# Kernel optimization log

Measured on AMD Instinct MI355X. Metric: run time of the kernel, lower is better.

## Reference

```python
import jax, jax.numpy as jnp
import numpy as np

B, L, D_IN = 16384, 28, 256
LATENT, HID = 128, 256
STEP = 0.5  # odeint rk4 step_size
N_STEPS = 2 * (L - 1)  # 54 fixed-grid steps covering t in [0, 27]


def setup_inputs() -> dict:
    key = jax.random.key(0)
    ks = jax.random.split(key, 20)
    s = 0.1  # init std used in ODEFunc; reuse for all params for simplicity
    p = {}
    p["trajectory"] = jax.random.normal(ks[0], (B, L, D_IN), dtype=jnp.float32)
    # encoder: Linear(3*D_IN -> HID), Linear(HID -> LATENT)
    p["We1"] = jax.random.normal(ks[1], (HID, 3 * D_IN)) * s
    p["be1"] = jnp.zeros((HID,))
    p["We2"] = jax.random.normal(ks[2], (LATENT, HID)) * s
    p["be2"] = jnp.zeros((LATENT,))
    # ODEFunc time embed: Linear(1 -> LATENT) -> vector form
    p["wte"] = jax.random.normal(ks[3], (LATENT,)) * s
    p["bte"] = jnp.zeros((LATENT,))
    # ODEFunc net: LATENT -> HID -> HID -> LATENT
    p["W1"] = jax.random.normal(ks[4], (HID, LATENT)) * s
    p["b1"] = jnp.zeros((HID,))
    p["W2"] = jax.random.normal(ks[5], (HID, HID)) * s
    p["b2"] = jnp.zeros((HID,))
    p["W3"] = jax.random.normal(ks[6], (LATENT, HID)) * s
    p["b3"] = jnp.zeros((LATENT,))
    # classifier: LATENT -> HID -> 1
    p["Wc1"] = jax.random.normal(ks[7], (HID, LATENT)) * s
    p["bc1"] = jnp.zeros((HID,))
    p["Wc2"] = jax.random.normal(ks[8], (1, HID)) * s
    p["bc2"] = jnp.zeros((1,))
    return p


def _forward(trajectory, We1, be1, We2, be2, wte, bte, W1, b1, W2, b2, W3, b3,
             Wc1, bc1, Wc2, bc2):
    bsz = trajectory.shape[0]
    # encoder (eval mode: dropout is identity)
    x0 = trajectory[:, :3, :].reshape(bsz, -1)  # [B, 3*D_IN]
    h = jax.nn.relu(x0 @ We1.T + be1)
    z0 = h @ We2.T + be2  # [B, LATENT]

    def f(t, z):
        # z + time embedding, then 3-layer tanh MLP
        zt = z + (t * wte + bte)
        h1 = jnp.tanh(zt @ W1.T + b1)
        h2 = jnp.tanh(h1 @ W2.T + b2)
        return h2 @ W3.T + b3

    def rk4_step(z, n):
        # torchdiffeq 'rk4' fixed-grid = 3/8-rule RK4
        t = n.astype(z.dtype) * STEP
        dt = jnp.asarray(STEP, z.dtype)
        k1 = f(t, z)
        k2 = f(t + dt / 3, z + dt * k1 / 3)
        k3 = f(t + 2 * dt / 3, z + dt * (k2 - k1 / 3))
        k4 = f(t + dt, z + dt * (k1 - k2 + k3))
        z_new = z + dt * (k1 + 3 * (k2 + k3) + k4) / 8
        return z_new, z_new

    _, zs = jax.lax.scan(rk4_step, z0, jnp.arange(N_STEPS))  # [54, B, LATENT]
    # output grid t = 0,1,...,27: z0 plus every second substep state
    z_trajectory = jnp.concatenate([z0[None], zs[1::2]], axis=0)  # [28, B, LATENT]

    zL = z_trajectory[-1]
    hc = jax.nn.relu(zL @ Wc1.T + bc1)
    prob = jax.nn.sigmoid(hc @ Wc2.T + bc2)  # [B, 1]
    return prob, z_trajectory


def reference(trajectory, We1, be1, We2, be2, wte, bte, W1, b1, W2, b2, W3, b3,
              Wc1, bc1, Wc2, bc2):
    return _forward(trajectory, We1, be1, We2, be2, wte, bte, W1, b1, W2, b2,
                    W3, b3, Wc1, bc1, Wc2, bc2)
```

## Files before the change

### kernel.cpp

```cpp
#include <hip/hip_runtime.h>
#include <cstdint>
#include <cstddef>

#define DEV __device__ __forceinline__

typedef float  f32x2  __attribute__((ext_vector_type(2)));
typedef float  f32x4  __attribute__((ext_vector_type(4)));
typedef float  f32x16 __attribute__((ext_vector_type(16)));
typedef int    i32x2  __attribute__((ext_vector_type(2)));
typedef int    i32x4  __attribute__((ext_vector_type(4)));
typedef _Float16 f16x2 __attribute__((ext_vector_type(2)));
typedef _Float16 f16x8 __attribute__((ext_vector_type(8)));

constexpr float DT   = 0.5f;
constexpr float DT3  = 0.5f / 3.0f;
constexpr float DT23 = 1.0f / 3.0f;
constexpr float DT8  = 0.0625f;

constexpr float S5  = 32.0f,   IS5 = 1.0f / 32.0f;
constexpr float S6  = 64.0f,   IS6 = 1.0f / 64.0f;
constexpr float S8  = 256.0f,  IS8 = 1.0f / 256.0f;
constexpr float S11 = 2048.0f;

constexpr int ACT  = 0;
constexpr int SLO  = 16384;
constexpr int ALO  = 32768;
constexpr int W2L  = 49152;
constexpr int W3L  = 114688;
constexpr int B2O  = 147456;
constexpr int B3O  = 148480;
constexpr int U01O = 148992;
constexpr int SMEM_BYTES = 151040;

#define MFMA16(a, b, c) __builtin_amdgcn_mfma_f32_32x32x16_f16((a), (b), (c), 0, 0, 0)

DEV int swzb(int off, int m) { return off ^ ((m & 7) << 4); }

DEV float tanh_fast(float x) {
  float e = __builtin_amdgcn_exp2f(x * 2.885390082f);
  return 1.0f - 2.0f * __builtin_amdgcn_rcpf(e + 1.0f);
}

DEV unsigned pkh2(float a, float b) {
  f16x2 p = { (_Float16)a, (_Float16)b };
  return __builtin_bit_cast(unsigned, p);
}

DEV f16x8 read_f16t(const char* buf, int RS, int m, int kelem) {
  return *(const f16x8*)(buf + swzb(m * RS + kelem * 2, m));
}
DEV i32x2 read8b(const char* buf, int m, int kelem) {
  return *(const i32x2*)(buf + swzb(m * 256 + kelem, m));
}
DEV f16x8 mulh(f16x8 v, float s) {
  _Float16 h = (_Float16)s;
  f16x8 r;
#pragma unroll
  for (int j = 0; j < 8; ++j) r[j] = v[j] * h;
  return r;
}
DEV f16x8 dec8(i32x2 r, float sc) {
  f32x2 p0 = __builtin_amdgcn_cvt_pk_f32_fp8(r[0], false);
  f32x2 p1 = __builtin_amdgcn_cvt_pk_f32_fp8(r[0], true);
  f32x2 p2 = __builtin_amdgcn_cvt_pk_f32_fp8(r[1], false);
  f32x2 p3 = __builtin_amdgcn_cvt_pk_f32_fp8(r[1], true);
  f16x2 q0 = __builtin_bit_cast(f16x2, __builtin_amdgcn_cvt_pkrtz(p0[0] * sc, p0[1] * sc));
  f16x2 q1 = __builtin_bit_cast(f16x2, __builtin_amdgcn_cvt_pkrtz(p1[0] * sc, p1[1] * sc));
  f16x2 q2 = __builtin_bit_cast(f16x2, __builtin_amdgcn_cvt_pkrtz(p2[0] * sc, p2[1] * sc));
  f16x2 q3 = __builtin_bit_cast(f16x2, __builtin_amdgcn_cvt_pkrtz(p3[0] * sc, p3[1] * sc));
  f16x8 o;
  o[0] = q0[0]; o[1] = q0[1]; o[2] = q1[0]; o[3] = q1[1];
  o[4] = q2[0]; o[5] = q2[1]; o[6] = q3[0]; o[7] = q3[1];
  return o;
}
DEV int pk4fp8(float a, float b, float c, float d) {
  int w = __builtin_amdgcn_cvt_pk_fp8_f32(a, b, 0, false);
  w = __builtin_amdgcn_cvt_pk_fp8_f32(c, d, w, true);
  return w;
}

DEV void cvt_hl_s(const float* p, f16x8& hi, f16x8& lo, float ls) {
  f32x4 a = *(const f32x4*)p;
  f32x4 b = *(const f32x4*)(p + 4);
#pragma unroll
  for (int j = 0; j < 4; ++j) {
    _Float16 h = (_Float16)a[j]; hi[j] = h; lo[j] = (_Float16)((a[j] - (float)h) * ls);
    _Float16 g = (_Float16)b[j]; hi[4 + j] = g; lo[4 + j] = (_Float16)((b[j] - (float)g) * ls);
  }
}
DEV f16x8 cvt_h(const float* p) {
  f32x4 a = *(const f32x4*)p;
  f32x4 b = *(const f32x4*)(p + 4);
  f16x8 hi;
#pragma unroll
  for (int j = 0; j < 4; ++j) { hi[j] = (_Float16)a[j]; hi[4 + j] = (_Float16)b[j]; }
  return hi;
}
DEV f16x8 cvt8v(f32x4 a, f32x4 b) {
  f16x8 h;
#pragma unroll
  for (int j = 0; j < 4; ++j) { h[j] = (_Float16)a[j]; h[4 + j] = (_Float16)b[j]; }
  return h;
}

DEV void write_h8(char* hi, char* lo, f32x16 acc[2][2], int lane, int nbase) {
  const int mr = lane & 31, hh = lane >> 5;
#pragma unroll
  for (int nt = 0; nt < 2; ++nt)
#pragma unroll
    for (int mt = 0; mt < 2; ++mt) {
      int m = mt * 32 + mr;
#pragma unroll
      for (int g = 0; g < 4; ++g) {
        int n = nbase + nt * 32 + 8 * g + 4 * hh;
        float v0 = tanh_fast(acc[nt][mt][4 * g + 0]);
        float v1 = tanh_fast(acc[nt][mt][4 * g + 1]);
        float v2 = tanh_fast(acc[nt][mt][4 * g + 2]);
        float v3 = tanh_fast(acc[nt][mt][4 * g + 3]);
        i32x2 w;
        w[0] = (int)pkh2(v0, v1);
        w[1] = (int)pkh2(v2, v3);
        *(i32x2*)(hi + swzb(m * 512 + n * 2, m)) = w;
        float l0 = (v0 - (float)(_Float16)v0) * S11;
        float l1 = (v1 - (float)(_Float16)v1) * S11;
        float l2 = (v2 - (float)(_Float16)v2) * S11;
        float l3 = (v3 - (float)(_Float16)v3) * S11;
        *(int*)(lo + swzb(m * 256 + n, m)) = pk4fp8(l0, l1, l2, l3);
      }
    }
}

DEV void write_h16(char* hi, char* lo, f32x16 acc[2][2], int lane, int nbase, float ls) {
  const int mr = lane & 31, hh = lane >> 5;
#pragma unroll
  for (int nt = 0; nt < 2; ++nt)
#pragma unroll
    for (int mt = 0; mt < 2; ++mt) {
      int m = mt * 32 + mr;
#pragma unroll
      for (int g = 0; g < 4; ++g) {
        int n = nbase + nt * 32 + 8 * g + 4 * hh;
        float v0 = fmaxf(acc[nt][mt][4 * g + 0], 0.f);
        float v1 = fmaxf(acc[nt][mt][4 * g + 1], 0.f);
        float v2 = fmaxf(acc[nt][mt][4 * g + 2], 0.f);
        float v3 = fmaxf(acc[nt][mt][4 * g + 3], 0.f);
        i32x2 w;
        w[0] = (int)pkh2(v0, v1); w[1] = (int)pkh2(v2, v3);
        *(i32x2*)(hi + swzb(m * 512 + n * 2, m)) = w;
        w[0] = (int)pkh2((v0 - (float)(_Float16)v0) * ls, (v1 - (float)(_Float16)v1) * ls);
        w[1] = (int)pkh2((v2 - (float)(_Float16)v2) * ls, (v3 - (float)(_Float16)v3) * ls);
        *(i32x2*)(lo + swzb(m * 512 + n * 2, m)) = w;
      }
    }
}

DEV void write_hc(char* hi, f32x16 acc[2][2], int lane, int nbase) {
  const int mr = lane & 31, hh = lane >> 5;
#pragma unroll
  for (int nt = 0; nt < 2; ++nt)
#pragma unroll
    for (int mt = 0; mt < 2; ++mt) {
      int m = mt * 32 + mr;
#pragma unroll
      for (int g = 0; g < 4; ++g) {
        int n = nbase + nt * 32 + 8 * g + 4 * hh;
        i32x2 w;
        w[0] = (int)pkh2(fmaxf(acc[nt][mt][4 * g + 0], 0.f), fmaxf(acc[nt][mt][4 * g + 1], 0.f));
        w[1] = (int)pkh2(fmaxf(acc[nt][mt][4 * g + 2], 0.f), fmaxf(acc[nt][mt][4 * g + 3], 0.f));
        *(i32x2*)(hi + swzb(m * 512 + n * 2, m)) = w;
      }
    }
}

DEV void write_f32v(char* dst, const f32x16& a0, const f32x16& a1, int lane, int nbase) {
  const int mr = lane & 31, hh = lane >> 5;
#pragma unroll
  for (int mt = 0; mt < 2; ++mt) {
    const f32x16& a = mt ? a1 : a0;
    int m = mt * 32 + mr;
#pragma unroll
    for (int g = 0; g < 4; ++g) {
      int n = nbase + 8 * g + 4 * hh;
      f32x4 v = { a[4 * g + 0], a[4 * g + 1], a[4 * g + 2], a[4 * g + 3] };
      *(f32x4*)(dst + swzb(m * 512 + n * 4, m)) = v;
    }
  }
}

DEV void read_kv(const char* sm, int m, int cs, float* kv) {
#pragma unroll
  for (int blk = 0; blk < 8; ++blk) {
    f32x4 v = *(const f32x4*)(sm + ACT + swzb(m * 512 + cs * 128 + blk * 16, m));
    kv[4 * blk] = v[0]; kv[4 * blk + 1] = v[1]; kv[4 * blk + 2] = v[2]; kv[4 * blk + 3] = v[3];
  }
}

DEV void write_stage8(char* sm, int m, int cs, int gg, const float* sv) {
  i32x4 wh, wl;
#pragma unroll
  for (int j = 0; j < 4; ++j) {
    float v0 = sv[2 * j], v1 = sv[2 * j + 1];
    _Float16 h0 = (_Float16)v0, h1 = (_Float16)v1;
    f16x2 ph = { h0, h1 };
    f16x2 pl = { (_Float16)((v0 - (float)h0) * S5), (_Float16)((v1 - (float)h1) * S5) };
    wh[j] = __builtin_bit_cast(int, ph);
    wl[j] = __builtin_bit_cast(int, pl);
  }
  int off = swzb(m * 256 + cs * 64 + gg * 16, m);
  *(i32x4*)(sm + ACT + off) = wh;
  *(i32x4*)(sm + SLO + off) = wl;
}

DEV void f_eval(char* sm, const f16x8* wsW1, float t,
                const f16x8* W1h, const f16x8* Au,
                const float* __restrict__ W2, const float* __restrict__ W3,
                int lane, int wave) {
  const int mr = lane & 31, kh = (lane >> 5) * 8, hh = lane >> 5;
  const int wb64 = wave * 64, wb32 = wave * 32;

  __syncthreads();
  f32x16 a1[2][2];
#pragma unroll
  for (int nt = 0; nt < 2; ++nt)
#pragma unroll
    for (int mt = 0; mt < 2; ++mt)
#pragma unroll
      for (int r = 0; r < 16; ++r) a1[nt][mt][r] = 0.f;

  const f16x8* wp = wsW1 + (size_t)wave * 1024 + lane;
  f16x8 wq[2][2];
  wq[0][0] = wp[0];   wq[0][1] = wp[512];
  wq[1][0] = wp[64];  wq[1][1] = wp[512 + 64];
#pragma unroll
  for (int ks = 0; ks < 8; ++ks) {
    f16x8 wl0 = wq[ks & 1][0], wl1 = wq[ks & 1][1];
    if (ks + 2 < 8) {
      wq[ks & 1][0] = wp[(ks + 2) * 64];
      wq[ks & 1][1] = wp[512 + (ks + 2) * 64];
    }
    int ke = ks * 16 + kh;
    f16x8 bh0 = read_f16t(sm + ACT, 256, mr, ke);
    f16x8 bh1 = read_f16t(sm + ACT, 256, 32 + mr, ke);
    f16x8 bl0 = read_f16t(sm + SLO, 256, mr, ke);
    f16x8 bl1 = read_f16t(sm + SLO, 256, 32 + mr, ke);
    f16x8 bh0m = mulh(bh0, IS8), bh1m = mulh(bh1, IS8);
    f16x8 w1s0 = mulh(W1h[ks], IS5), w1s1 = mulh(W1h[8 + ks], IS5);
    a1[0][0] = MFMA16(W1h[ks],     bh0, a1[0][0]);
    a1[0][1] = MFMA16(W1h[ks],     bh1, a1[0][1]);
    a1[1][0] = MFMA16(W1h[8 + ks], bh0, a1[1][0]);
    a1[1][1] = MFMA16(W1h[8 + ks], bh1, a1[1][1]);
    a1[0][0] = MFMA16(w1s0, bl0, a1[0][0]);
    a1[0][1] = MFMA16(w1s0, bl1, a1[0][1]);
    a1[1][0] = MFMA16(w1s1, bl0, a1[1][0]);
    a1[1][1] = MFMA16(w1s1, bl1, a1[1][1]);
    a1[0][0] = MFMA16(wl0, bh0m, a1[0][0]);
    a1[0][1] = MFMA16(wl0, bh1m, a1[0][1]);
    a1[1][0] = MFMA16(wl1, bh0m, a1[1][0]);
    a1[1][1] = MFMA16(wl1, bh1m, a1[1][1]);
  }
  {
    _Float16 th = (_Float16)t;
    _Float16 tl = (_Float16)(t - (float)th);
    f16x8 ub, ul;
#pragma unroll
    for (int j = 0; j < 8; ++j) { ub[j] = (_Float16)0.f; ul[j] = (_Float16)0.f; }
    if (kh == 0) {
      ub[0] = (_Float16)1.0f; ub[1] = th;
      ub[2] = (_Float16)IS8;  ub[3] = (_Float16)((float)th * IS8);
      ul[1] = tl;             ul[3] = (_Float16)((float)tl * IS8);
    }
#pragma unroll
    for (int nt = 0; nt < 2; ++nt) {
      a1[nt][0] = MFMA16(Au[nt], ub, a1[nt][0]);
      a1[nt][1] = MFMA16(Au[nt], ub, a1[nt][1]);
      a1[nt][0] = MFMA16(Au[nt], ul, a1[nt][0]);
      a1[nt][1] = MFMA16(Au[nt], ul, a1[nt][1]);
    }
  }
  __syncthreads();
  write_h8(sm + ACT, sm + ALO, a1, lane, wb64);
  __syncthreads();

  const float* B2p = (const float*)(sm + B2O);
  f32x16 a2[2][2];
#pragma unroll
  for (int nt = 0; nt < 2; ++nt)
#pragma unroll
    for (int g = 0; g < 4; ++g) {
      int n = wb64 + nt * 32 + 8 * g + 4 * hh;
      f32x4 bv = *(const f32x4*)(B2p + n);
#pragma unroll
      for (int r = 0; r < 4; ++r) { a2[nt][0][4 * g + r] = bv[r]; a2[nt][1][4 * g + r] = bv[r]; }
    }
  const float* w2r0 = W2 + (size_t)(wb64 + mr) * 256 + kh;
  const float* w2r1 = W2 + (size_t)(wb64 + 32 + mr) * 256 + kh;
  f32x4 w2b[2][2][2];
#pragma unroll
  for (int s = 0; s < 2; ++s) {
    w2b[s][0][0] = *(const f32x4*)(w2r0 + s * 16);
    w2b[s][0][1] = *(const f32x4*)(w2r0 + s * 16 + 4);
    w2b[s][1][0] = *(const f32x4*)(w2r1 + s * 16);
    w2b[s][1][1] = *(const f32x4*)(w2r1 + s * 16 + 4);
  }
#pragma unroll
  for (int ks = 0; ks < 16; ++ks) {
    f16x8 W2h0 = cvt8v(w2b[ks & 1][0][0], w2b[ks & 1][0][1]);
    f16x8 W2h1 = cvt8v(w2b[ks & 1][1][0], w2b[ks & 1][1][1]);
    if (ks + 2 < 16) {
      w2b[ks & 1][0][0] = *(const f32x4*)(w2r0 + (ks + 2) * 16);
      w2b[ks & 1][0][1] = *(const f32x4*)(w2r0 + (ks + 2) * 16 + 4);
      w2b[ks & 1][1][0] = *(const f32x4*)(w2r1 + (ks + 2) * 16);
      w2b[ks & 1][1][1] = *(const f32x4*)(w2r1 + (ks + 2) * 16 + 4);
    }
    int ke = ks * 16 + kh;
    f16x8 bh0 = read_f16t(sm + ACT, 512, mr, ke);
    f16x8 bh1 = read_f16t(sm + ACT, 512, 32 + mr, ke);
    f16x8 bl0 = dec8(read8b(sm + ALO, mr, ke), IS6);
    f16x8 bl1 = dec8(read8b(sm + ALO, 32 + mr, ke), IS6);
    f16x8 w2s0 = mulh(W2h0, IS5), w2s1 = mulh(W2h1, IS5);
    f16x8 bh0m = mulh(bh0, IS6), bh1m = mulh(bh1, IS6);
    i32x2 t0 = *(const i32x2*)(sm + W2L + ((size_t)((wave * 2 + 0) * 16 + ks) * 64 + lane) * 8);
    i32x2 t1 = *(const i32x2*)(sm + W2L + ((size_t)((wave * 2 + 1) * 16 + ks) * 64 + lane) * 8);
    f16x8 wa0 = dec8(t0, IS5), wa1 = dec8(t1, IS5);
    a2[0][0] = MFMA16(W2h0, bh0, a2[0][0]);
    a2[0][1] = MFMA16(W2h0, bh1, a2[0][1]);
    a2[1][0] = MFMA16(W2h1, bh0, a2[1][0]);
    a2[1][1] = MFMA16(W2h1, bh1, a2[1][1]);
    a2[0][0] = MFMA16(w2s0, bl0, a2[0][0]);
    a2[0][1] = MFMA16(w2s0, bl1, a2[0][1]);
    a2[1][0] = MFMA16(w2s1, bl0, a2[1][0]);
    a2[1][1] = MFMA16(w2s1, bl1, a2[1][1]);
    a2[0][0] = MFMA16(wa0, bh0m, a2[0][0]);
    a2[0][1] = MFMA16(wa0, bh1m, a2[0][1]);
    a2[1][0] = MFMA16(wa1, bh0m, a2[1][0]);
    a2[1][1] = MFMA16(wa1, bh1m, a2[1][1]);
  }
  __syncthreads();
  write_h8(sm + ACT, sm + ALO, a2, lane, wb64);
  __syncthreads();

  const float* B3p = (const float*)(sm + B3O);
  f32x16 a30, a31;
#pragma unroll
  for (int g = 0; g < 4; ++g) {
    int n = wb32 + 8 * g + 4 * hh;
    f32x4 bv = *(const f32x4*)(B3p + n);
#pragma unroll
    for (int r = 0; r < 4; ++r) { a30[4 * g + r] = bv[r]; a31[4 * g + r] = bv[r]; }
  }
  const float* w3r = W3 + (size_t)(wb32 + mr) * 256 + kh;
  f32x4 w3b[2][2];
#pragma unroll
  for (int s = 0; s < 2; ++s) {
    w3b[s][0] = *(const f32x4*)(w3r + s * 16);
    w3b[s][1] = *(const f32x4*)(w3r + s * 16 + 4);
  }
#pragma unroll
  for (int ks = 0; ks < 16; ++ks) {
    f16x8 W3h = cvt8v(w3b[ks & 1][0], w3b[ks & 1][1]);
    if (ks + 2 < 16) {
      w3b[ks & 1][0] = *(const f32x4*)(w3r + (ks + 2) * 16);
      w3b[ks & 1][1] = *(const f32x4*)(w3r + (ks + 2) * 16 + 4);
    }
    int ke = ks * 16 + kh;
    f16x8 bh0 = read_f16t(sm + ACT, 512, mr, ke);
    f16x8 bh1 = read_f16t(sm + ACT, 512, 32 + mr, ke);
    f16x8 bl0 = dec8(read8b(sm + ALO, mr, ke), IS6);
    f16x8 bl1 = dec8(read8b(sm + ALO, 32 + mr, ke), IS6);
    f16x8 w3s = mulh(W3h, IS5);
    f16x8 bh0m = mulh(bh0, IS6), bh1m = mulh(bh1, IS6);
    i32x2 t0 = *(const i32x2*)(sm + W3L + ((size_t)(wave * 16 + ks) * 64 + lane) * 8);
    f16x8 wa = dec8(t0, IS5);
    a30 = MFMA16(W3h, bh0, a30);
    a31 = MFMA16(W3h, bh1, a31);
    a30 = MFMA16(w3s, bl0, a30);
    a31 = MFMA16(w3s, bl1, a31);
    a30 = MFMA16(wa, bh0m, a30);
    a31 = MFMA16(wa, bh1m, a31);
  }
  __syncthreads();
  write_f32v(sm + ACT, a30, a31, lane, wb32);
  __syncthreads();
}

__global__ void prep_w1lo(const float* __restrict__ W1, _Float16* __restrict__ ws) {
  int i = blockIdx.x * 256 + threadIdx.x;
  int lane = i & 63, ks = (i >> 6) & 7, nt = (i >> 9) & 1, wave = (i >> 10) & 3;
  int row = wave * 64 + nt * 32 + (lane & 31);
  int col = ks * 16 + (lane >> 5) * 8;
  const float* p = W1 + (size_t)row * 128 + col;
  _Float16* o = ws + (size_t)i * 8;
#pragma unroll
  for (int j = 0; j < 8; ++j) {
    float w = p[j];
    _Float16 h = (_Float16)w;
    o[j] = (_Float16)((w - (float)h) * S8);
  }
}

__global__ __launch_bounds__(256, 1) void node_kernel(
    const float* __restrict__ traj,
    const float* __restrict__ We1, const float* __restrict__ be1,
    const float* __restrict__ We2, const float* __restrict__ be2,
    const float* __restrict__ wte, const float* __restrict__ bte,
    const float* __restrict__ W1,  const float* __restrict__ b1,
    const float* __restrict__ W2,  const float* __restrict__ b2,
    const float* __restrict__ W3,  const float* __restrict__ b3,
    const float* __restrict__ Wc1, const float* __restrict__ bc1,
    const float* __restrict__ Wc2, const float* __restrict__ bc2,
    const _Float16* __restrict__ wsW1h, float* __restrict__ out) {
  __shared__ __align__(16) char sm[SMEM_BYTES];
  const int tid  = threadIdx.x;
  const int lane = tid & 63, wave = tid >> 6;
  const int mr = lane & 31, kh = (lane >> 5) * 8, hh = lane >> 5;
  const int wb64 = wave * 64, wb32 = wave * 32;
  const int brow = blockIdx.x * 64;
  const f16x8* wsW1 = (const f16x8*)wsW1h;

  {
    int n = tid;
    float u0 = b1[n], u1 = 0.f;
    const float* wr = W1 + n * 128;
    for (int k = 0; k < 128; ++k) { float w = wr[k]; u1 += wte[k] * w; u0 += bte[k] * w; }
    float* U = (float*)(sm + U01O);
    U[2 * n] = u0; U[2 * n + 1] = u1;
    ((float*)(sm + B2O))[n] = b2[n];
    if (n < 128) ((float*)(sm + B3O))[n] = b3[n];
  }

  f16x8 W1h[16], Au[2];
#pragma unroll
  for (int nt = 0; nt < 2; ++nt)
#pragma unroll
    for (int ks = 0; ks < 8; ++ks)
      W1h[nt * 8 + ks] = cvt_h(W1 + (size_t)(wb64 + nt * 32 + mr) * 128 + ks * 16 + kh);

  __syncthreads();

#pragma unroll
  for (int nt = 0; nt < 2; ++nt) {
    f16x8 a;
#pragma unroll
    for (int j = 0; j < 8; ++j) a[j] = (_Float16)0.f;
    if (kh == 0) {
      const float* U = (const float*)(sm + U01O);
      int n = wb64 + nt * 32 + mr;
      float u0 = U[2 * n], u1 = U[2 * n + 1];
      _Float16 u0h = (_Float16)u0, u1h = (_Float16)u1;
      a[0] = u0h; a[1] = u1h;
      a[2] = (_Float16)((u0 - (float)u0h) * S8);
      a[3] = (_Float16)((u1 - (float)u1h) * S8);
    }
    Au[nt] = a;
  }

  const int m_own = tid >> 2, cs = tid & 3;

  f32x16 ae[2][2];
#pragma unroll
  for (int nt = 0; nt < 2; ++nt)
#pragma unroll
    for (int mt = 0; mt < 2; ++mt)
#pragma unroll
      for (int r = 0; r < 16; ++r) ae[nt][mt][r] = 0.f;

  for (int c = 0; c < 3; ++c) {
#pragma unroll
    for (int g = 0; g < 8; ++g) {
      const float* xp = traj + (size_t)(brow + m_own) * 7168 + c * 256 + cs * 64 + g * 8;
      f32x4 a = *(const f32x4*)xp;
      f32x4 b = *(const f32x4*)(xp + 4);
      i32x4 wh, wl;
#pragma unroll
      for (int j = 0; j < 2; ++j) {
        float v0 = a[2 * j], v1 = a[2 * j + 1];
        _Float16 h0 = (_Float16)v0, h1 = (_Float16)v1;
        f16x2 ph = { h0, h1 };
        f16x2 pl = { (_Float16)((v0 - (float)h0) * S6), (_Float16)((v1 - (float)h1) * S6) };
        wh[j] = __builtin_bit_cast(int, ph); wl[j] = __builtin_bit_cast(int, pl);
        float w0 = b[2 * j], w1 = b[2 * j + 1];
        _Float16 g0 = (_Float16)w0, g1 = (_Float16)w1;
        f16x2 qh = { g0, g1 };
        f16x2 ql = { (_Float16)((w0 - (float)g0) * S6), (_Float16)((w1 - (float)g1) * S6) };
        wh[2 + j] = __builtin_bit_cast(int, qh); wl[2 + j] = __builtin_bit_cast(int, ql);
      }
      int off = swzb(m_own * 512 + cs * 128 + g * 16, m_own);
      *(i32x4*)(sm + ACT + off) = wh;
      *(i32x4*)(sm + W2L + off) = wl;
    }
    __syncthreads();
#pragma unroll
    for (int ks = 0; ks < 16; ++ks) {
      int ke = ks * 16 + kh;
      f16x8 bh0 = read_f16t(sm + ACT, 512, mr, ke);
      f16x8 bh1 = read_f16t(sm + ACT, 512, 32 + mr, ke);
      f16x8 bl0 = read_f16t(sm + W2L, 512, mr, ke);
      f16x8 bl1 = read_f16t(sm + W2L, 512, 32 + mr, ke);
      f16x8 bh0m = mulh(bh0, IS6), bh1m = mulh(bh1, IS6);
#pragma unroll
      for (int nt = 0; nt < 2; ++nt) {
        f16x8 wh, wl;
        cvt_hl_s(We1 + (size_t)(wb64 + nt * 32 + mr) * 768 + c * 256 + ks * 16 + kh, wh, wl, S6);
        f16x8 whs = mulh(wh, IS6);
        ae[nt][0] = MFMA16(wh, bh0, ae[nt][0]);
        ae[nt][1] = MFMA16(wh, bh1, ae[nt][1]);
        ae[nt][0] = MFMA16(whs, bl0, ae[nt][0]);
        ae[nt][1] = MFMA16(whs, bl1, ae[nt][1]);
        ae[nt][0] = MFMA16(wl, bh0m, ae[nt][0]);
        ae[nt][1] = MFMA16(wl, bh1m, ae[nt][1]);
      }
    }
    __syncthreads();
  }
#pragma unroll
  for (int nt = 0; nt < 2; ++nt)
#pragma unroll
    for (int r = 0; r < 16; ++r) {
      int n = wb64 + nt * 32 + (r & 3) + 8 * (r >> 2) + 4 * hh;
      float bv = be1[n];
      ae[nt][0][r] += bv; ae[nt][1][r] += bv;
    }
  write_h16(sm + ACT, sm + W2L, ae, lane, wb64, S6);
  __syncthreads();

  {
    f32x16 az0, az1;
#pragma unroll
    for (int r = 0; r < 16; ++r) { az0[r] = 0.f; az1[r] = 0.f; }
#pragma unroll
    for (int ks = 0; ks < 16; ++ks) {
      int ke = ks * 16 + kh;
      f16x8 bh0 = read_f16t(sm + ACT, 512, mr, ke);
      f16x8 bh1 = read_f16t(sm + ACT, 512, 32 + mr, ke);
      f16x8 bl0 = read_f16t(sm + W2L, 512, mr, ke);
      f16x8 bl1 = read_f16t(sm + W2L, 512, 32 + mr, ke);
      f16x8 bh0m = mulh(bh0, IS6), bh1m = mulh(bh1, IS6);
      f16x8 wh, wl;
      cvt_hl_s(We2 + (size_t)(wb32 + mr) * 256 + ks * 16 + kh, wh, wl, S6);
      f16x8 whs = mulh(wh, IS6);
      az0 = MFMA16(wh, bh0, az0);
      az1 = MFMA16(wh, bh1, az1);
      az0 = MFMA16(whs, bl0, az0);
      az1 = MFMA16(whs, bl1, az1);
      az0 = MFMA16(wl, bh0m, az0);
      az1 = MFMA16(wl, bh1m, az1);
    }
#pragma unroll
    for (int r = 0; r < 16; ++r) {
      int n = wb32 + (r & 3) + 8 * (r >> 2) + 4 * hh;
      float bv = be2[n];
      az0[r] += bv; az1[r] += bv;
    }
    __syncthreads();
    write_f32v(sm + ACT, az0, az1, lane, wb32);
    __syncthreads();
  }

  float z[32], Acc[32], k1v[32], kv[32];
  read_kv(sm, m_own, cs, z);
  float* outz = out + 16384;
  {
    float* p = outz + (size_t)(brow + m_own) * 128 + cs * 32;
#pragma unroll
    for (int g = 0; g < 8; ++g) {
      f32x4 v = { z[4 * g], z[4 * g + 1], z[4 * g + 2], z[4 * g + 3] };
      *(f32x4*)(p + 4 * g) = v;
    }
  }

#pragma unroll
  for (int nt = 0; nt < 2; ++nt)
    for (int ks = 0; ks < 16; ++ks) {
      const float* p = W2 + (size_t)(wb64 + nt * 32 + mr) * 256 + ks * 16 + kh;
      float l[8];
#pragma unroll
      for (int j = 0; j < 8; ++j) { float w = p[j]; l[j] = (w - (float)(_Float16)w) * S11; }
      i32x2 wv;
      wv[0] = pk4fp8(l[0], l[1], l[2], l[3]);
      wv[1] = pk4fp8(l[4], l[5], l[6], l[7]);
      *(i32x2*)(sm + W2L + ((size_t)((wave * 2 + nt) * 16 + ks) * 64 + lane) * 8) = wv;
    }
  for (int ks = 0; ks < 16; ++ks) {
    const float* p = W3 + (size_t)(wb32 + mr) * 256 + ks * 16 + kh;
    float l[8];
#pragma unroll
    for (int j = 0; j < 8; ++j) { float w = p[j]; l[j] = (w - (float)(_Float16)w) * S11; }
    i32x2 wv;
    wv[0] = pk4fp8(l[0], l[1], l[2], l[3]);
    wv[1] = pk4fp8(l[4], l[5], l[6], l[7]);
    *(i32x2*)(sm + W3L + ((size_t)(wave * 16 + ks) * 64 + lane) * 8) = wv;
  }

  for (int st = 0; st < 54; ++st) {
    float t0 = st * 0.5f;
    __syncthreads();
#pragma unroll
    for (int gg = 0; gg < 4; ++gg) write_stage8(sm, m_own, cs, gg, z + 8 * gg);
    f_eval(sm, wsW1, t0, W1h, Au, W2, W3, lane, wave);
    read_kv(sm, m_own, cs, kv);
    __syncthreads();
#pragma unroll
    for (int gg = 0; gg < 4; ++gg) {
      float sv[8];
#pragma unroll
      for (int i = 0; i < 8; ++i) {
        int e = 8 * gg + i;
        Acc[e] = z[e] + DT8 * kv[e];
        sv[i] = z[e] + DT3 * kv[e];
        k1v[e] = kv[e];
      }
      write_stage8(sm, m_own, cs, gg, sv);
    }
    f_eval(sm, wsW1, t0 + DT3, W1h, Au, W2, W3, lane, wave);
    read_kv(sm, m_own, cs, kv);
    __syncthreads();
#pragma unroll
    for (int gg = 0; gg < 4; ++gg) {
      float sv[8];
#pragma unroll
      for (int i = 0; i < 8; ++i) {
        int e = 8 * gg + i;
        Acc[e] += 3.0f * DT8 * kv[e];
        sv[i] = z[e] + DT * kv[e] - DT3 * k1v[e];
        k1v[e] = k1v[e] - kv[e];
      }
      write_stage8(sm, m_own, cs, gg, sv);
    }
    f_eval(sm, wsW1, t0 + DT23, W1h, Au, W2, W3, lane, wave);
    read_kv(sm, m_own, cs, kv);
    __syncthreads();
#pragma unroll
    for (int gg = 0; gg < 4; ++gg) {
      float sv[8];
#pragma unroll
      for (int i = 0; i < 8; ++i) {
        int e = 8 * gg + i;
        Acc[e] += 3.0f * DT8 * kv[e];
        sv[i] = z[e] + DT * (k1v[e] + kv[e]);
      }
      write_stage8(sm, m_own, cs, gg, sv);
    }
    f_eval(sm, wsW1, t0 + DT, W1h, Au, W2, W3, lane, wave);
    read_kv(sm, m_own, cs, kv);
#pragma unroll
    for (int e = 0; e < 32; ++e) z[e] = Acc[e] + DT8 * kv[e];
    if (st & 1) {
      int frame = (st >> 1) + 1;
      float* p = outz + (size_t)frame * 2097152 + (size_t)(brow + m_own) * 128 + cs * 32;
#pragma unroll
      for (int g = 0; g < 8; ++g) {
        f32x4 v = { z[4 * g], z[4 * g + 1], z[4 * g + 2], z[4 * g + 3] };
        *(f32x4*)(p + 4 * g) = v;
      }
    }
  }

  __syncthreads();
#pragma unroll
  for (int gg = 0; gg < 4; ++gg) write_stage8(sm, m_own, cs, gg, z + 8 * gg);
  __syncthreads();
  f32x16 ac[2][2];
#pragma unroll
  for (int nt = 0; nt < 2; ++nt)
#pragma unroll
    for (int r = 0; r < 16; ++r) {
      int n = wb64 + nt * 32 + (r & 3) + 8 * (r >> 2) + 4 * hh;
      float bv = bc1[n];
      ac[nt][0][r] = bv; ac[nt][1][r] = bv;
    }
#pragma unroll
  for (int ks = 0; ks < 8; ++ks) {
    int ke = ks * 16 + kh;
    f16x8 bh0 = read_f16t(sm + ACT, 256, mr, ke);
    f16x8 bh1 = read_f16t(sm + ACT, 256, 32 + mr, ke);
    f16x8 bl0 = read_f16t(sm + SLO, 256, mr, ke);
    f16x8 bl1 = read_f16t(sm + SLO, 256, 32 + mr, ke);
#pragma unroll
    for (int nt = 0; nt < 2; ++nt) {
      f16x8 wh, wl;
      cvt_hl_s(Wc1 + (size_t)(wb64 + nt * 32 + mr) * 128 + ks * 16 + kh, wh, wl, 1.0f);
      f16x8 whs = mulh(wh, IS5);
      ac[nt][0] = MFMA16(wh, bh0, ac[nt][0]);
      ac[nt][1] = MFMA16(wh, bh1, ac[nt][1]);
      ac[nt][0] = MFMA16(whs, bl0, ac[nt][0]);
      ac[nt][1] = MFMA16(whs, bl1, ac[nt][1]);
      ac[nt][0] = MFMA16(wl, bh0, ac[nt][0]);
      ac[nt][1] = MFMA16(wl, bh1, ac[nt][1]);
    }
  }
  __syncthreads();
  write_hc(sm + ACT, ac, lane, wb64);
  __syncthreads();
  if (tid < 64) {
    float acc = bc2[0];
#pragma unroll 8
    for (int c0 = 0; c0 < 256; c0 += 8) {
      f16x8 hv = read_f16t(sm + ACT, 512, tid, c0);
#pragma unroll
      for (int j = 0; j < 8; ++j) acc += (float)hv[j] * Wc2[c0 + j];
    }
    out[brow + tid] = __builtin_amdgcn_rcpf(1.0f + __builtin_amdgcn_exp2f(-acc * 1.442695041f));
  }
}

extern "C" void kernel_launch(void* const* d_in, const int* in_sizes, int n_in,
                              void* d_out, int out_size, void* d_ws, size_t ws_size,
                              hipStream_t stream) {
  (void)in_sizes; (void)n_in; (void)out_size; (void)ws_size;
  const float* traj = (const float*)d_in[0];
  const float* We1  = (const float*)d_in[1];
  const float* be1  = (const float*)d_in[2];
  const float* We2  = (const float*)d_in[3];
  const float* be2  = (const float*)d_in[4];
  const float* wte  = (const float*)d_in[5];
  const float* bte  = (const float*)d_in[6];
  const float* W1   = (const float*)d_in[7];
  const float* b1   = (const float*)d_in[8];
  const float* W2   = (const float*)d_in[9];
  const float* b2   = (const float*)d_in[10];
  const float* W3   = (const float*)d_in[11];
  const float* b3   = (const float*)d_in[12];
  const float* Wc1  = (const float*)d_in[13];
  const float* bc1  = (const float*)d_in[14];
  const float* Wc2  = (const float*)d_in[15];
  const float* bc2  = (const float*)d_in[16];
  _Float16* wsW1 = (_Float16*)d_ws;
  hipLaunchKernelGGL(prep_w1lo, dim3(16), dim3(256), 0, stream, W1, wsW1);
  hipLaunchKernelGGL(node_kernel, dim3(256), dim3(256), 0, stream,
                     traj, We1, be1, We2, be2, wte, bte, W1, b1, W2, b2, W3, b3,
                     Wc1, bc1, Wc2, bc2, (const _Float16*)wsW1, (float*)d_out);
}
```

Before: 7.953 ms.

## Precompute split-precision W1/W2/W3 tables in workspace and spill RK4 state to LDS

A prep kernel now pre-splits W1, W2 and W3 into fp16 high and scaled low (fp16 or fp8) parts in MFMA fragment order in the global workspace. f_eval loads these directly instead of converting fp32 weights every step or keeping W1 in registers and the W2/W3 low parts in LDS. The RK4 accumulator and k1 state move from registers to LDS, which cuts register pressure. The LDS swizzle mask is widened to 31 or 15 depending on row stride to reduce bank conflicts. In exchange the kernel reads more weight bytes from global or L2 per step and does extra LDS traffic for the RK4 state.

After: 10.39 ms. 1.31x slower.

```diff
diff --git a/kernel.cpp b/kernel.cpp
--- a/kernel.cpp
+++ b/kernel.cpp
@@ -14,7 +14,6 @@
 
 constexpr float DT   = 0.5f;
 constexpr float DT3  = 0.5f / 3.0f;
-constexpr float DT23 = 1.0f / 3.0f;
 constexpr float DT8  = 0.0625f;
 
 constexpr float S5  = 32.0f,   IS5 = 1.0f / 32.0f;
@@ -25,16 +24,23 @@
 constexpr int ACT  = 0;
 constexpr int SLO  = 16384;
 constexpr int ALO  = 32768;
-constexpr int W2L  = 49152;
-constexpr int W3L  = 114688;
-constexpr int B2O  = 147456;
-constexpr int B3O  = 148480;
-constexpr int U01O = 148992;
-constexpr int SMEM_BYTES = 151040;
+constexpr int ACCS = 49152;
+constexpr int K1SO = 81920;
+constexpr int B2O  = 114688;
+constexpr int B3O  = 115712;
+constexpr int U01O = 116224;
+constexpr int SMEM_BYTES = 118272;
+
+constexpr int WS_W1H = 0;
+constexpr int WS_W1L = 65536;
+constexpr int WS_W2H = 131072;
+constexpr int WS_W2L = 262144;
+constexpr int WS_W3H = 327680;
+constexpr int WS_W3L = 393216;
 
 #define MFMA16(a, b, c) __builtin_amdgcn_mfma_f32_32x32x16_f16((a), (b), (c), 0, 0, 0)
 
-DEV int swzb(int off, int m) { return off ^ ((m & 7) << 4); }
+DEV int swz(int off, int m, int mask) { return off ^ ((m & mask) << 4); }
 
 DEV float tanh_fast(float x) {
   float e = __builtin_amdgcn_exp2f(x * 2.885390082f);
@@ -46,11 +52,11 @@
   return __builtin_bit_cast(unsigned, p);
 }
 
-DEV f16x8 read_f16t(const char* buf, int RS, int m, int kelem) {
-  return *(const f16x8*)(buf + swzb(m * RS + kelem * 2, m));
+DEV f16x8 read_f16t(const char* buf, int RS, int m, int kelem, int mask) {
+  return *(const f16x8*)(buf + swz(m * RS + kelem * 2, m, mask));
 }
 DEV i32x2 read8b(const char* buf, int m, int kelem) {
-  return *(const i32x2*)(buf + swzb(m * 256 + kelem, m));
+  return *(const i32x2*)(buf + swz(m * 256 + kelem, m, 15));
 }
 DEV f16x8 mulh(f16x8 v, float s) {
   _Float16 h = (_Float16)s;
@@ -88,20 +94,6 @@
     _Float16 g = (_Float16)b[j]; hi[4 + j] = g; lo[4 + j] = (_Float16)((b[j] - (float)g) * ls);
   }
 }
-DEV f16x8 cvt_h(const float* p) {
-  f32x4 a = *(const f32x4*)p;
-  f32x4 b = *(const f32x4*)(p + 4);
-  f16x8 hi;
-#pragma unroll
-  for (int j = 0; j < 4; ++j) { hi[j] = (_Float16)a[j]; hi[4 + j] = (_Float16)b[j]; }
-  return hi;
-}
-DEV f16x8 cvt8v(f32x4 a, f32x4 b) {
-  f16x8 h;
-#pragma unroll
-  for (int j = 0; j < 4; ++j) { h[j] = (_Float16)a[j]; h[4 + j] = (_Float16)b[j]; }
-  return h;
-}
 
 DEV void write_h8(char* hi, char* lo, f32x16 acc[2][2], int lane, int nbase) {
   const int mr = lane & 31, hh = lane >> 5;
@@ -120,12 +112,12 @@
         i32x2 w;
         w[0] = (int)pkh2(v0, v1);
         w[1] = (int)pkh2(v2, v3);
-        *(i32x2*)(hi + swzb(m * 512 + n * 2, m)) = w;
+        *(i32x2*)(hi + swz(m * 512 + n * 2, m, 31)) = w;
         float l0 = (v0 - (float)(_Float16)v0) * S11;
         float l1 = (v1 - (float)(_Float16)v1) * S11;
         float l2 = (v2 - (float)(_Float16)v2) * S11;
         float l3 = (v3 - (float)(_Float16)v3) * S11;
-        *(int*)(lo + swzb(m * 256 + n, m)) = pk4fp8(l0, l1, l2, l3);
+        *(int*)(lo + swz(m * 256 + n, m, 15)) = pk4fp8(l0, l1, l2, l3);
       }
     }
 }
@@ -146,10 +138,10 @@
         float v3 = fmaxf(acc[nt][mt][4 * g + 3], 0.f);
         i32x2 w;
         w[0] = (int)pkh2(v0, v1); w[1] = (int)pkh2(v2, v3);
-        *(i32x2*)(hi + swzb(m * 512 + n * 2, m)) = w;
+        *(i32x2*)(hi + swz(m * 512 + n * 2, m, 31)) = w;
         w[0] = (int)pkh2((v0 - (float)(_Float16)v0) * ls, (v1 - (float)(_Float16)v1) * ls);
         w[1] = (int)pkh2((v2 - (float)(_Float16)v2) * ls, (v3 - (float)(_Float16)v3) * ls);
-        *(i32x2*)(lo + swzb(m * 512 + n * 2, m)) = w;
+        *(i32x2*)(lo + swz(m * 512 + n * 2, m, 31)) = w;
       }
     }
 }
@@ -167,7 +159,7 @@
         i32x2 w;
         w[0] = (int)pkh2(fmaxf(acc[nt][mt][4 * g + 0], 0.f), fmaxf(acc[nt][mt][4 * g + 1], 0.f));
         w[1] = (int)pkh2(fmaxf(acc[nt][mt][4 * g + 2], 0.f), fmaxf(acc[nt][mt][4 * g + 3], 0.f));
-        *(i32x2*)(hi + swzb(m * 512 + n * 2, m)) = w;
+        *(i32x2*)(hi + swz(m * 512 + n * 2, m, 31)) = w;
       }
     }
 }
@@ -182,7 +174,7 @@
     for (int g = 0; g < 4; ++g) {
       int n = nbase + 8 * g + 4 * hh;
       f32x4 v = { a[4 * g + 0], a[4 * g + 1], a[4 * g + 2], a[4 * g + 3] };
-      *(f32x4*)(dst + swzb(m * 512 + n * 4, m)) = v;
+      *(f32x4*)(dst + swz(m * 512 + n * 4, m, 31)) = v;
     }
   }
 }
@@ -190,9 +182,16 @@
 DEV void read_kv(const char* sm, int m, int cs, float* kv) {
 #pragma unroll
   for (int blk = 0; blk < 8; ++blk) {
-    f32x4 v = *(const f32x4*)(sm + ACT + swzb(m * 512 + cs * 128 + blk * 16, m));
+    f32x4 v = *(const f32x4*)(sm + ACT + swz(m * 512 + cs * 128 + blk * 16, m, 31));
     kv[4 * blk] = v[0]; kv[4 * blk + 1] = v[1]; kv[4 * blk + 2] = v[2]; kv[4 * blk + 3] = v[3];
   }
+}
+
+DEV f32x4 ld_st(const char* sm, int base, int m, int cs, int g) {
+  return *(const f32x4*)(sm + base + swz(m * 512 + cs * 128 + g * 16, m, 31));
+}
+DEV void st_st(char* sm, int base, int m, int cs, int g, f32x4 v) {
+  *(f32x4*)(sm + base + swz(m * 512 + cs * 128 + g * 16, m, 31)) = v;
 }
 
 DEV void write_stage8(char* sm, int m, int cs, int gg, const float* sv) {
@@ -206,17 +205,20 @@
     wh[j] = __builtin_bit_cast(int, ph);
     wl[j] = __builtin_bit_cast(int, pl);
   }
-  int off = swzb(m * 256 + cs * 64 + gg * 16, m);
+  int off = swz(m * 256 + cs * 64 + gg * 16, m, 15);
   *(i32x4*)(sm + ACT + off) = wh;
   *(i32x4*)(sm + SLO + off) = wl;
 }
 
-DEV void f_eval(char* sm, const f16x8* wsW1, float t,
-                const f16x8* W1h, const f16x8* Au,
-                const float* __restrict__ W2, const float* __restrict__ W3,
-                int lane, int wave) {
+DEV void f_eval(char* sm, const char* ws, float t, const f16x8* Au, int lane, int wave) {
   const int mr = lane & 31, kh = (lane >> 5) * 8, hh = lane >> 5;
   const int wb64 = wave * 64, wb32 = wave * 32;
+  const f16x8* W1H = (const f16x8*)(ws + WS_W1H) + wave * 1024 + lane;
+  const f16x8* W1L = (const f16x8*)(ws + WS_W1L) + wave * 1024 + lane;
+  const f16x8* W2H = (const f16x8*)(ws + WS_W2H) + wave * 2048 + lane;
+  const i32x2* W2Lo = (const i32x2*)(ws + WS_W2L) + wave * 2048 + lane;
+  const f16x8* W3H = (const f16x8*)(ws + WS_W3H) + wave * 1024 + lane;
+  const i32x2* W3Lo = (const i32x2*)(ws + WS_W3L) + wave * 1024 + lane;
 
   __syncthreads();
   f32x16 a1[2][2];
@@ -227,36 +229,36 @@
 #pragma unroll
       for (int r = 0; r < 16; ++r) a1[nt][mt][r] = 0.f;
 
-  const f16x8* wp = wsW1 + (size_t)wave * 1024 + lane;
-  f16x8 wq[2][2];
-  wq[0][0] = wp[0];   wq[0][1] = wp[512];
-  wq[1][0] = wp[64];  wq[1][1] = wp[512 + 64];
+  f16x8 wh[2][2], wl[2][2];
+  wh[0][0] = W1H[0];  wh[0][1] = W1H[512];      wl[0][0] = W1L[0];  wl[0][1] = W1L[512];
+  wh[1][0] = W1H[64]; wh[1][1] = W1H[512 + 64]; wl[1][0] = W1L[64]; wl[1][1] = W1L[512 + 64];
 #pragma unroll
   for (int ks = 0; ks < 8; ++ks) {
-    f16x8 wl0 = wq[ks & 1][0], wl1 = wq[ks & 1][1];
+    f16x8 h0 = wh[ks & 1][0], h1 = wh[ks & 1][1];
+    f16x8 l0 = wl[ks & 1][0], l1 = wl[ks & 1][1];
     if (ks + 2 < 8) {
-      wq[ks & 1][0] = wp[(ks + 2) * 64];
-      wq[ks & 1][1] = wp[512 + (ks + 2) * 64];
+      wh[ks & 1][0] = W1H[(ks + 2) * 64]; wh[ks & 1][1] = W1H[512 + (ks + 2) * 64];
+      wl[ks & 1][0] = W1L[(ks + 2) * 64]; wl[ks & 1][1] = W1L[512 + (ks + 2) * 64];
     }
     int ke = ks * 16 + kh;
-    f16x8 bh0 = read_f16t(sm + ACT, 256, mr, ke);
-    f16x8 bh1 = read_f16t(sm + ACT, 256, 32 + mr, ke);
-    f16x8 bl0 = read_f16t(sm + SLO, 256, mr, ke);
-    f16x8 bl1 = read_f16t(sm + SLO, 256, 32 + mr, ke);
+    f16x8 bh0 = read_f16t(sm + ACT, 256, mr, ke, 15);
+    f16x8 bh1 = read_f16t(sm + ACT, 256, 32 + mr, ke, 15);
+    f16x8 bl0 = read_f16t(sm + SLO, 256, mr, ke, 15);
+    f16x8 bl1 = read_f16t(sm + SLO, 256, 32 + mr, ke, 15);
     f16x8 bh0m = mulh(bh0, IS8), bh1m = mulh(bh1, IS8);
-    f16x8 w1s0 = mulh(W1h[ks], IS5), w1s1 = mulh(W1h[8 + ks], IS5);
-    a1[0][0] = MFMA16(W1h[ks],     bh0, a1[0][0]);
-    a1[0][1] = MFMA16(W1h[ks],     bh1, a1[0][1]);
-    a1[1][0] = MFMA16(W1h[8 + ks], bh0, a1[1][0]);
-    a1[1][1] = MFMA16(W1h[8 + ks], bh1, a1[1][1]);
+    f16x8 w1s0 = mulh(h0, IS5), w1s1 = mulh(h1, IS5);
+    a1[0][0] = MFMA16(h0, bh0, a1[0][0]);
+    a1[0][1] = MFMA16(h0, bh1, a1[0][1]);
+    a1[1][0] = MFMA16(h1, bh0, a1[1][0]);
+    a1[1][1] = MFMA16(h1, bh1, a1[1][1]);
     a1[0][0] = MFMA16(w1s0, bl0, a1[0][0]);
     a1[0][1] = MFMA16(w1s0, bl1, a1[0][1]);
     a1[1][0] = MFMA16(w1s1, bl0, a1[1][0]);
     a1[1][1] = MFMA16(w1s1, bl1, a1[1][1]);
-    a1[0][0] = MFMA16(wl0, bh0m, a1[0][0]);
-    a1[0][1] = MFMA16(wl0, bh1m, a1[0][1]);
-    a1[1][0] = MFMA16(wl1, bh0m, a1[1][0]);
-    a1[1][1] = MFMA16(wl1, bh1m, a1[1][1]);
+    a1[0][0] = MFMA16(l0, bh0m, a1[0][0]);
+    a1[0][1] = MFMA16(l0, bh1m, a1[0][1]);
+    a1[1][0] = MFMA16(l1, bh0m, a1[1][0]);
+    a1[1][1] = MFMA16(l1, bh1m, a1[1][1]);
   }
   {
     _Float16 th = (_Float16)t;
@@ -292,35 +294,24 @@
 #pragma unroll
       for (int r = 0; r < 4; ++r) { a2[nt][0][4 * g + r] = bv[r]; a2[nt][1][4 * g + r] = bv[r]; }
     }
-  const float* w2r0 = W2 + (size_t)(wb64 + mr) * 256 + kh;
-  const float* w2r1 = W2 + (size_t)(wb64 + 32 + mr) * 256 + kh;
-  f32x4 w2b[2][2][2];
-#pragma unroll
-  for (int s = 0; s < 2; ++s) {
-    w2b[s][0][0] = *(const f32x4*)(w2r0 + s * 16);
-    w2b[s][0][1] = *(const f32x4*)(w2r0 + s * 16 + 4);
-    w2b[s][1][0] = *(const f32x4*)(w2r1 + s * 16);
-    w2b[s][1][1] = *(const f32x4*)(w2r1 + s * 16 + 4);
-  }
+  f16x8 w2h[2][2]; i32x2 w2l[2][2];
+  w2h[0][0] = W2H[0];  w2h[0][1] = W2H[1024];      w2l[0][0] = W2Lo[0];  w2l[0][1] = W2Lo[1024];
+  w2h[1][0] = W2H[64]; w2h[1][1] = W2H[1024 + 64]; w2l[1][0] = W2Lo[64]; w2l[1][1] = W2Lo[1024 + 64];
 #pragma unroll
   for (int ks = 0; ks < 16; ++ks) {
-    f16x8 W2h0 = cvt8v(w2b[ks & 1][0][0], w2b[ks & 1][0][1]);
-    f16x8 W2h1 = cvt8v(w2b[ks & 1][1][0], w2b[ks & 1][1][1]);
+    f16x8 W2h0 = w2h[ks & 1][0], W2h1 = w2h[ks & 1][1];
+    i32x2 t0 = w2l[ks & 1][0], t1 = w2l[ks & 1][1];
     if (ks + 2 < 16) {
-      w2b[ks & 1][0][0] = *(const f32x4*)(w2r0 + (ks + 2) * 16);
-      w2b[ks & 1][0][1] = *(const f32x4*)(w2r0 + (ks + 2) * 16 + 4);
-      w2b[ks & 1][1][0] = *(const f32x4*)(w2r1 + (ks + 2) * 16);
-      w2b[ks & 1][1][1] = *(const f32x4*)(w2r1 + (ks + 2) * 16 + 4);
+      w2h[ks & 1][0] = W2H[(ks + 2) * 64];  w2h[ks & 1][1] = W2H[1024 + (ks + 2) * 64];
+      w2l[ks & 1][0] = W2Lo[(ks + 2) * 64]; w2l[ks & 1][1] = W2Lo[1024 + (ks + 2) * 64];
     }
     int ke = ks * 16 + kh;
-    f16x8 bh0 = read_f16t(sm + ACT, 512, mr, ke);
-    f16x8 bh1 = read_f16t(sm + ACT, 512, 32 + mr, ke);
+    f16x8 bh0 = read_f16t(sm + ACT, 512, mr, ke, 31);
+    f16x8 bh1 = read_f16t(sm + ACT, 512, 32 + mr, ke, 31);
     f16x8 bl0 = dec8(read8b(sm + ALO, mr, ke), IS6);
     f16x8 bl1 = dec8(read8b(sm + ALO, 32 + mr, ke), IS6);
     f16x8 w2s0 = mulh(W2h0, IS5), w2s1 = mulh(W2h1, IS5);
     f16x8 bh0m = mulh(bh0, IS6), bh1m = mulh(bh1, IS6);
-    i32x2 t0 = *(const i32x2*)(sm + W2L + ((size_t)((wave * 2 + 0) * 16 + ks) * 64 + lane) * 8);
-    i32x2 t1 = *(const i32x2*)(sm + W2L + ((size_t)((wave * 2 + 1) * 16 + ks) * 64 + lane) * 8);
     f16x8 wa0 = dec8(t0, IS5), wa1 = dec8(t1, IS5);
     a2[0][0] = MFMA16(W2h0, bh0, a2[0][0]);
     a2[0][1] = MFMA16(W2h0, bh1, a2[0][1]);
@@ -348,28 +339,23 @@
 #pragma unroll
     for (int r = 0; r < 4; ++r) { a30[4 * g + r] = bv[r]; a31[4 * g + r] = bv[r]; }
   }
-  const float* w3r = W3 + (size_t)(wb32 + mr) * 256 + kh;
-  f32x4 w3b[2][2];
-#pragma unroll
-  for (int s = 0; s < 2; ++s) {
-    w3b[s][0] = *(const f32x4*)(w3r + s * 16);
-    w3b[s][1] = *(const f32x4*)(w3r + s * 16 + 4);
-  }
+  f16x8 w3h[2]; i32x2 w3l[2];
+  w3h[0] = W3H[0]; w3h[1] = W3H[64]; w3l[0] = W3Lo[0]; w3l[1] = W3Lo[64];
 #pragma unroll
   for (int ks = 0; ks < 16; ++ks) {
-    f16x8 W3h = cvt8v(w3b[ks & 1][0], w3b[ks & 1][1]);
+    f16x8 W3h = w3h[ks & 1];
+    i32x2 t0 = w3l[ks & 1];
     if (ks + 2 < 16) {
-      w3b[ks & 1][0] = *(const f32x4*)(w3r + (ks + 2) * 16);
-      w3b[ks & 1][1] = *(const f32x4*)(w3r + (ks + 2) * 16 + 4);
+      w3h[ks & 1] = W3H[(ks + 2) * 64];
+      w3l[ks & 1] = W3Lo[(ks + 2) * 64];
     }
     int ke = ks * 16 + kh;
-    f16x8 bh0 = read_f16t(sm + ACT, 512, mr, ke);
-    f16x8 bh1 = read_f16t(sm + ACT, 512, 32 + mr, ke);
+    f16x8 bh0 = read_f16t(sm + ACT, 512, mr, ke, 31);
+    f16x8 bh1 = read_f16t(sm + ACT, 512, 32 + mr, ke, 31);
     f16x8 bl0 = dec8(read8b(sm + ALO, mr, ke), IS6);
     f16x8 bl1 = dec8(read8b(sm + ALO, 32 + mr, ke), IS6);
     f16x8 w3s = mulh(W3h, IS5);
     f16x8 bh0m = mulh(bh0, IS6), bh1m = mulh(bh1, IS6);
-    i32x2 t0 = *(const i32x2*)(sm + W3L + ((size_t)(wave * 16 + ks) * 64 + lane) * 8);
     f16x8 wa = dec8(t0, IS5);
     a30 = MFMA16(W3h, bh0, a30);
     a31 = MFMA16(W3h, bh1, a31);
@@ -383,18 +369,53 @@
   __syncthreads();
 }
 
-__global__ void prep_w1lo(const float* __restrict__ W1, _Float16* __restrict__ ws) {
+__global__ void prep_tabs(const float* __restrict__ W1, const float* __restrict__ W2,
+                          const float* __restrict__ W3, char* __restrict__ ws) {
   int i = blockIdx.x * 256 + threadIdx.x;
-  int lane = i & 63, ks = (i >> 6) & 7, nt = (i >> 9) & 1, wave = (i >> 10) & 3;
-  int row = wave * 64 + nt * 32 + (lane & 31);
-  int col = ks * 16 + (lane >> 5) * 8;
-  const float* p = W1 + (size_t)row * 128 + col;
-  _Float16* o = ws + (size_t)i * 8;
-#pragma unroll
-  for (int j = 0; j < 8; ++j) {
-    float w = p[j];
-    _Float16 h = (_Float16)w;
-    o[j] = (_Float16)((w - (float)h) * S8);
+  int lane = i & 63, mr = lane & 31, kh = (lane >> 5) * 8;
+  {
+    int ks = (i >> 6) & 15, nt = (i >> 10) & 1, wave = (i >> 11) & 3;
+    const float* p = W2 + (size_t)(wave * 64 + nt * 32 + mr) * 256 + ks * 16 + kh;
+    f16x8 hi; float l[8];
+#pragma unroll
+    for (int j = 0; j < 8; ++j) {
+      float w = p[j]; _Float16 h = (_Float16)w;
+      hi[j] = h; l[j] = (w - (float)h) * S11;
+    }
+    *(f16x8*)(ws + WS_W2H + (size_t)i * 16) = hi;
+    i32x2 wv;
+    wv[0] = pk4fp8(l[0], l[1], l[2], l[3]);
+    wv[1] = pk4fp8(l[4], l[5], l[6], l[7]);
+    *(i32x2*)(ws + WS_W2L + (size_t)i * 8) = wv;
+  }
+  if (i < 4096) {
+    {
+      int ks = (i >> 6) & 7, nt = (i >> 9) & 1, wave = (i >> 10) & 3;
+      const float* p = W1 + (size_t)(wave * 64 + nt * 32 + mr) * 128 + ks * 16 + kh;
+      f16x8 hi, lo;
+#pragma unroll
+      for (int j = 0; j < 8; ++j) {
+        float w = p[j]; _Float16 h = (_Float16)w;
+        hi[j] = h; lo[j] = (_Float16)((w - (float)h) * S8);
+      }
+      *(f16x8*)(ws + WS_W1H + (size_t)i * 16) = hi;
+      *(f16x8*)(ws + WS_W1L + (size_t)i * 16) = lo;
+    }
+    {
+      int ks = (i >> 6) & 15, wave = (i >> 10) & 3;
+      const float* p = W3 + (size_t)(wave * 32 + mr) * 256 + ks * 16 + kh;
+      f16x8 hi; float l[8];
+#pragma unroll
+      for (int j = 0; j < 8; ++j) {
+        float w = p[j]; _Float16 h = (_Float16)w;
+        hi[j] = h; l[j] = (w - (float)h) * S11;
+      }
+      *(f16x8*)(ws + WS_W3H + (size_t)i * 16) = hi;
+      i32x2 wv;
+      wv[0] = pk4fp8(l[0], l[1], l[2], l[3]);
+      wv[1] = pk4fp8(l[4], l[5], l[6], l[7]);
+      *(i32x2*)(ws + WS_W3L + (size_t)i * 8) = wv;
+    }
   }
 }
 
@@ -408,14 +429,13 @@
     const float* __restrict__ W3,  const float* __restrict__ b3,
     const float* __restrict__ Wc1, const float* __restrict__ bc1,
     const float* __restrict__ Wc2, const float* __restrict__ bc2,
-    const _Float16* __restrict__ wsW1h, float* __restrict__ out) {
+    const char* __restrict__ ws, float* __restrict__ out) {
   __shared__ __align__(16) char sm[SMEM_BYTES];
   const int tid  = threadIdx.x;
   const int lane = tid & 63, wave = tid >> 6;
   const int mr = lane & 31, kh = (lane >> 5) * 8, hh = lane >> 5;
   const int wb64 = wave * 64, wb32 = wave * 32;
   const int brow = blockIdx.x * 64;
-  const f16x8* wsW1 = (const f16x8*)wsW1h;
 
   {
     int n = tid;
@@ -427,16 +447,9 @@
     ((float*)(sm + B2O))[n] = b2[n];
     if (n < 128) ((float*)(sm + B3O))[n] = b3[n];
   }
-
-  f16x8 W1h[16], Au[2];
-#pragma unroll
-  for (int nt = 0; nt < 2; ++nt)
-#pragma unroll
-    for (int ks = 0; ks < 8; ++ks)
-      W1h[nt * 8 + ks] = cvt_h(W1 + (size_t)(wb64 + nt * 32 + mr) * 128 + ks * 16 + kh);
-
-  __syncthreads();
-
+  __syncthreads();
+
+  f16x8 Au[2];
 #pragma unroll
   for (int nt = 0; nt < 2; ++nt) {
     f16x8 a;
@@ -484,18 +497,18 @@
         f16x2 ql = { (_Float16)((w0 - (float)g0) * S6), (_Float16)((w1 - (float)g1) * S6) };
         wh[2 + j] = __builtin_bit_cast(int, qh); wl[2 + j] = __builtin_bit_cast(int, ql);
       }
-      int off = swzb(m_own * 512 + cs * 128 + g * 16, m_own);
+      int off = swz(m_own * 512 + cs * 128 + g * 16, m_own, 31);
       *(i32x4*)(sm + ACT + off) = wh;
-      *(i32x4*)(sm + W2L + off) = wl;
+      *(i32x4*)(sm + ACCS + off) = wl;
     }
     __syncthreads();
 #pragma unroll
     for (int ks = 0; ks < 16; ++ks) {
       int ke = ks * 16 + kh;
-      f16x8 bh0 = read_f16t(sm + ACT, 512, mr, ke);
-      f16x8 bh1 = read_f16t(sm + ACT, 512, 32 + mr, ke);
-      f16x8 bl0 = read_f16t(sm + W2L, 512, mr, ke);
-      f16x8 bl1 = read_f16t(sm + W2L, 512, 32 + mr, ke);
+      f16x8 bh0 = read_f16t(sm + ACT, 512, mr, ke, 31);
+      f16x8 bh1 = read_f16t(sm + ACT, 512, 32 + mr, ke, 31);
+      f16x8 bl0 = read_f16t(sm + ACCS, 512, mr, ke, 31);
+      f16x8 bl1 = read_f16t(sm + ACCS, 512, 32 + mr, ke, 31);
       f16x8 bh0m = mulh(bh0, IS6), bh1m = mulh(bh1, IS6);
 #pragma unroll
       for (int nt = 0; nt < 2; ++nt) {
@@ -520,7 +533,7 @@
       float bv = be1[n];
       ae[nt][0][r] += bv; ae[nt][1][r] += bv;
     }
-  write_h16(sm + ACT, sm + W2L, ae, lane, wb64, S6);
+  write_h16(sm + ACT, sm + ACCS, ae, lane, wb64, S6);
   __syncthreads();
 
   {
@@ -530,10 +543,10 @@
 #pragma unroll
     for (int ks = 0; ks < 16; ++ks) {
       int ke = ks * 16 + kh;
-      f16x8 bh0 = read_f16t(sm + ACT, 512, mr, ke);
-      f16x8 bh1 = read_f16t(sm + ACT, 512, 32 + mr, ke);
-      f16x8 bl0 = read_f16t(sm + W2L, 512, mr, ke);
-      f16x8 bl1 = read_f16t(sm + W2L, 512, 32 + mr, ke);
+      f16x8 bh0 = read_f16t(sm + ACT, 512, mr, ke, 31);
+      f16x8 bh1 = read_f16t(sm + ACT, 512, 32 + mr, ke, 31);
+      f16x8 bl0 = read_f16t(sm + ACCS, 512, mr, ke, 31);
+      f16x8 bl1 = read_f16t(sm + ACCS, 512, 32 + mr, ke, 31);
       f16x8 bh0m = mulh(bh0, IS6), bh1m = mulh(bh1, IS6);
       f16x8 wh, wl;
       cvt_hl_s(We2 + (size_t)(wb32 + mr) * 256 + ks * 16 + kh, wh, wl, S6);
@@ -556,7 +569,7 @@
     __syncthreads();
   }
 
-  float z[32], Acc[32], k1v[32], kv[32];
+  float z[32];
   read_kv(sm, m_own, cs, z);
   float* outz = out + 16384;
   {
@@ -568,82 +581,102 @@
     }
   }
 
-#pragma unroll
-  for (int nt = 0; nt < 2; ++nt)
-    for (int ks = 0; ks < 16; ++ks) {
-      const float* p = W2 + (size_t)(wb64 + nt * 32 + mr) * 256 + ks * 16 + kh;
-      float l[8];
-#pragma unroll
-      for (int j = 0; j < 8; ++j) { float w = p[j]; l[j] = (w - (float)(_Float16)w) * S11; }
-      i32x2 wv;
-      wv[0] = pk4fp8(l[0], l[1], l[2], l[3]);
-      wv[1] = pk4fp8(l[4], l[5], l[6], l[7]);
-      *(i32x2*)(sm + W2L + ((size_t)((wave * 2 + nt) * 16 + ks) * 64 + lane) * 8) = wv;
-    }
-  for (int ks = 0; ks < 16; ++ks) {
-    const float* p = W3 + (size_t)(wb32 + mr) * 256 + ks * 16 + kh;
-    float l[8];
-#pragma unroll
-    for (int j = 0; j < 8; ++j) { float w = p[j]; l[j] = (w - (float)(_Float16)w) * S11; }
-    i32x2 wv;
-    wv[0] = pk4fp8(l[0], l[1], l[2], l[3]);
-    wv[1] = pk4fp8(l[4], l[5], l[6], l[7]);
-    *(i32x2*)(sm + W3L + ((size_t)(wave * 16 + ks) * 64 + lane) * 8) = wv;
-  }
-
   for (int st = 0; st < 54; ++st) {
     float t0 = st * 0.5f;
     __syncthreads();
 #pragma unroll
     for (int gg = 0; gg < 4; ++gg) write_stage8(sm, m_own, cs, gg, z + 8 * gg);
-    f_eval(sm, wsW1, t0, W1h, Au, W2, W3, lane, wave);
-    read_kv(sm, m_own, cs, kv);
-    __syncthreads();
-#pragma unroll
-    for (int gg = 0; gg < 4; ++gg) {
-      float sv[8];
-#pragma unroll
-      for (int i = 0; i < 8; ++i) {
-        int e = 8 * gg + i;
-        Acc[e] = z[e] + DT8 * kv[e];
-        sv[i] = z[e] + DT3 * kv[e];
-        k1v[e] = kv[e];
-      }
-      write_stage8(sm, m_own, cs, gg, sv);
-    }
-    f_eval(sm, wsW1, t0 + DT3, W1h, Au, W2, W3, lane, wave);
-    read_kv(sm, m_own, cs, kv);
-    __syncthreads();
-#pragma unroll
-    for (int gg = 0; gg < 4; ++gg) {
-      float sv[8];
-#pragma unroll
-      for (int i = 0; i < 8; ++i) {
-        int e = 8 * gg + i;
-        Acc[e] += 3.0f * DT8 * kv[e];
-        sv[i] = z[e] + DT * kv[e] - DT3 * k1v[e];
-        k1v[e] = k1v[e] - kv[e];
-      }
-      write_stage8(sm, m_own, cs, gg, sv);
-    }
-    f_eval(sm, wsW1, t0 + DT23, W1h, Au, W2, W3, lane, wave);
-    read_kv(sm, m_own, cs, kv);
-    __syncthreads();
-#pragma unroll
-    for (int gg = 0; gg < 4; ++gg) {
-      float sv[8];
-#pragma unroll
-      for (int i = 0; i < 8; ++i) {
-        int e = 8 * gg + i;
-        Acc[e] += 3.0f * DT8 * kv[e];
-        sv[i] = z[e] + DT * (k1v[e] + kv[e]);
-      }
-      write_stage8(sm, m_own, cs, gg, sv);
-    }
-    f_eval(sm, wsW1, t0 + DT, W1h, Au, W2, W3, lane, wave);
-    read_kv(sm, m_own, cs, kv);
-#pragma unroll
-    for (int e = 0; e < 32; ++e) z[e] = Acc[e] + DT8 * kv[e];
+    f_eval(sm, ws, t0, Au, lane, wave);
+    {
+      float kv[32];
+      read_kv(sm, m_own, cs, kv);
+      __syncthreads();
+#pragma unroll
+      for (int gg = 0; gg < 4; ++gg) {
+        float sv[8];
+#pragma unroll
+        for (int h = 0; h < 2; ++h) {
+          int g = 2 * gg + h;
+          f32x4 k = { kv[4 * g], kv[4 * g + 1], kv[4 * g + 2], kv[4 * g + 3] };
+          f32x4 a, s;
+#pragma unroll
+          for (int j = 0; j < 4; ++j) {
+            int e = 4 * g + j;
+            a[j] = z[e] + DT8 * k[j];
+            s[j] = z[e] + DT3 * k[j];
+          }
+          st_st(sm, ACCS, m_own, cs, g, a);
+          st_st(sm, K1SO, m_own, cs, g, k);
+          sv[4 * h] = s[0]; sv[4 * h + 1] = s[1]; sv[4 * h + 2] = s[2]; sv[4 * h + 3] = s[3];
+        }
+        write_stage8(sm, m_own, cs, gg, sv);
+      }
+    }
+    f_eval(sm, ws, t0 + DT3, Au, lane, wave);
+    {
+      float kv[32];
+      read_kv(sm, m_own, cs, kv);
+      __syncthreads();
+#pragma unroll
+      for (int gg = 0; gg < 4; ++gg) {
+        float sv[8];
+#pragma unroll
+        for (int h = 0; h < 2; ++h) {
+          int g = 2 * gg + h;
+          f32x4 k1 = ld_st(sm, K1SO, m_own, cs, g);
+          f32x4 a  = ld_st(sm, ACCS, m_own, cs, g);
+          f32x4 d12, an;
+#pragma unroll
+          for (int j = 0; j < 4; ++j) {
+            int e = 4 * g + j;
+            float k2 = kv[e];
+            an[j] = a[j] + 3.0f * DT8 * k2;
+            sv[4 * h + j] = z[e] + DT * k2 - DT3 * k1[j];
+            d12[j] = k1[j] - k2;
+          }
+          st_st(sm, ACCS, m_own, cs, g, an);
+          st_st(sm, K1SO, m_own, cs, g, d12);
+        }
+        write_stage8(sm, m_own, cs, gg, sv);
+      }
+    }
+    f_eval(sm, ws, t0 + 2.0f * DT3, Au, lane, wave);
+    {
+      float kv[32];
+      read_kv(sm, m_own, cs, kv);
+      __syncthreads();
+#pragma unroll
+      for (int gg = 0; gg < 4; ++gg) {
+        float sv[8];
+#pragma unroll
+        for (int h = 0; h < 2; ++h) {
+          int g = 2 * gg + h;
+          f32x4 d12 = ld_st(sm, K1SO, m_own, cs, g);
+          f32x4 a   = ld_st(sm, ACCS, m_own, cs, g);
+          f32x4 an;
+#pragma unroll
+          for (int j = 0; j < 4; ++j) {
+            int e = 4 * g + j;
+            float k3 = kv[e];
+            an[j] = a[j] + 3.0f * DT8 * k3;
+            sv[4 * h + j] = z[e] + DT * (d12[j] + k3);
+          }
+          st_st(sm, ACCS, m_own, cs, g, an);
+        }
+        write_stage8(sm, m_own, cs, gg, sv);
+      }
+    }
+    f_eval(sm, ws, t0 + DT, Au, lane, wave);
+    {
+      float kv[32];
+      read_kv(sm, m_own, cs, kv);
+#pragma unroll
+      for (int g = 0; g < 8; ++g) {
+        f32x4 a = ld_st(sm, ACCS, m_own, cs, g);
+#pragma unroll
+        for (int j = 0; j < 4; ++j) z[4 * g + j] = a[j] + DT8 * kv[4 * g + j];
+      }
+    }
     if (st & 1) {
       int frame = (st >> 1) + 1;
       float* p = outz + (size_t)frame * 2097152 + (size_t)(brow + m_own) * 128 + cs * 32;
@@ -671,10 +704,10 @@
 #pragma unroll
   for (int ks = 0; ks < 8; ++ks) {
     int ke = ks * 16 + kh;
-    f16x8 bh0 = read_f16t(sm + ACT, 256, mr, ke);
-    f16x8 bh1 = read_f16t(sm + ACT, 256, 32 + mr, ke);
-    f16x8 bl0 = read_f16t(sm + SLO, 256, mr, ke);
-    f16x8 bl1 = read_f16t(sm + SLO, 256, 32 + mr, ke);
+    f16x8 bh0 = read_f16t(sm + ACT, 256, mr, ke, 15);
+    f16x8 bh1 = read_f16t(sm + ACT, 256, 32 + mr, ke, 15);
+    f16x8 bl0 = read_f16t(sm + SLO, 256, mr, ke, 15);
+    f16x8 bl1 = read_f16t(sm + SLO, 256, 32 + mr, ke, 15);
 #pragma unroll
     for (int nt = 0; nt < 2; ++nt) {
       f16x8 wh, wl;
@@ -695,7 +728,7 @@
     float acc = bc2[0];
 #pragma unroll 8
     for (int c0 = 0; c0 < 256; c0 += 8) {
-      f16x8 hv = read_f16t(sm + ACT, 512, tid, c0);
+      f16x8 hv = read_f16t(sm + ACT, 512, tid, c0, 31);
 #pragma unroll
       for (int j = 0; j < 8; ++j) acc += (float)hv[j] * Wc2[c0 + j];
     }
@@ -724,9 +757,9 @@
   const float* bc1  = (const float*)d_in[14];
   const float* Wc2  = (const float*)d_in[15];
   const float* bc2  = (const float*)d_in[16];
-  _Float16* wsW1 = (_Float16*)d_ws;
-  hipLaunchKernelGGL(prep_w1lo, dim3(16), dim3(256), 0, stream, W1, wsW1);
+  char* ws = (char*)d_ws;
+  hipLaunchKernelGGL(prep_tabs, dim3(32), dim3(256), 0, stream, W1, W2, W3, ws);
   hipLaunchKernelGGL(node_kernel, dim3(256), dim3(256), 0, stream,
                      traj, We1, be1, We2, be2, wte, bte, W1, b1, W2, b2, W3, b3,
-                     Wc1, bc1, Wc2, bc2, (const _Float16*)wsW1, (float*)d_out);
-}
+                     Wc1, bc1, Wc2, bc2, (const char*)ws, (float*)d_out);
+}
```
